# Optimization experiments

Measured on AMD Instinct MI355X. Metric: run time of the kernel, lower is better.

## Reference

```python
import jax, jax.numpy as jnp
import numpy as np

U = 8          # units per modular layer
B = 16384      # batch
IN = 512       # input feature dim
H = 512        # modular hidden dim
NC = 62        # n_class


def _aggregate(P, h):
    # P: [T, F] policy link matrix; h: [F, B, D] per-unit features.
    # agg[t] = sum_f P[t,f] * h[f], normalized by row-sum when row-sum > 0.
    s = jnp.einsum('tf,fbd->tbd', P, h)
    row = P.sum(axis=1)                      # [T]
    safe = jnp.where(row > 0, row, 1.0)[:, None, None]
    return jnp.where((row > 0)[:, None, None], s / safe, s)


def setup_inputs() -> dict:
    key = jax.random.key(0)
    ks = jax.random.split(key, 12)
    s_in = 1.0 / np.sqrt(IN)
    s_h = 1.0 / np.sqrt(H)
    return {
        'x': jax.random.normal(ks[0], (B, IN), jnp.float32),
        'policy1': jax.random.uniform(ks[1], (U * U,), jnp.float32),
        'policy2': jax.random.uniform(ks[2], (U * U,), jnp.float32),
        'policy_final': jax.random.uniform(ks[3], (U,), jnp.float32),
        'W0': jax.random.uniform(ks[4], (U, IN, H), jnp.float32, -s_in, s_in),
        'b0': jax.random.uniform(ks[5], (U, H), jnp.float32, -s_in, s_in),
        'W1': jax.random.uniform(ks[6], (U, H, H), jnp.float32, -s_h, s_h),
        'b1': jax.random.uniform(ks[7], (U, H), jnp.float32, -s_h, s_h),
        'W2': jax.random.uniform(ks[8], (U, H, NC), jnp.float32, -s_h, s_h),
        'b2': jax.random.uniform(ks[9], (U, NC), jnp.float32, -s_h, s_h),
    }


def reference(x, policy1, policy2, policy_final, W0, b0, W1, b1, W2, b2):
    # Layer 0 (input modular layer): policy_list[0] is forced to all-ones,
    # so every unit sees x unscaled. Each unit: Linear + ReLU.
    h0 = jax.nn.relu(jnp.einsum('bi,uid->ubd', x, W0) + b0[:, None, :])  # [U,B,H]

    # Mid layer: policy-gated weighted-sum aggregation, then per-unit Linear+ReLU.
    a1 = _aggregate(policy1.reshape(U, U), h0)
    h1 = jax.nn.relu(jnp.einsum('ubi,uid->ubd', a1, W1) + b1[:, None, :])

    # Output modular layer: aggregate then per-unit Linear (no activation).
    a2 = _aggregate(policy2.reshape(U, U), h1)
    h2 = jnp.einsum('ubi,uic->ubc', a2, W2) + b2[:, None, :]  # [U,B,NC]

    # Final gating. Original code divides by divider INSIDE the unit loop
    # (every iteration), so replicate that recurrence exactly.
    d = policy_final.sum()
    inv = jnp.where(d > 0, 1.0 / jnp.where(d > 0, d, 1.0), 1.0)
    out = jnp.zeros((B, NC), jnp.float32)
    for j in range(U):  # fixed small unit count, not a data dim
        out = (out + h2[j] * policy_final[j]) * inv
    return out
```

## Files before the change

kernel.cpp:

```cpp
#include <hip/hip_runtime.h>

#define U_   8
#define B_   16384
#define NC_  62

typedef __attribute__((ext_vector_type(8))) short bfrag;
typedef __attribute__((ext_vector_type(4))) float facc;

__device__ __forceinline__ float bf2f(unsigned int lo16) {
    union { unsigned int i; float f; } v;
    v.i = lo16 << 16;
    return v.f;
}
__device__ __forceinline__ unsigned short f2bf(float f) {
    unsigned int x = __float_as_uint(f);
    return (unsigned short)((x + 0x7fffu + ((x >> 16) & 1u)) >> 16);
}
__device__ __forceinline__ void gl2lds16(const void* g, void* l) {
    __builtin_amdgcn_global_load_lds(
        (const __attribute__((address_space(1))) void*)g,
        (__attribute__((address_space(3))) void*)l, 16, 0, 0);
}

__global__ void prep_kernel(const float* __restrict__ p1, const float* __restrict__ p2,
                            const float* __restrict__ pf, const float* __restrict__ b2,
                            float* __restrict__ P1n, float* __restrict__ P2n,
                            float* __restrict__ wfin, float* __restrict__ cconst)
{
    int t = threadIdx.x;
    if (t >= 64) return;
    int row = t >> 3;
    float s1 = 0.f, s2 = 0.f;
    for (int f = 0; f < 8; f++) { s1 += p1[row * 8 + f]; s2 += p2[row * 8 + f]; }
    P1n[t] = p1[t] * (s1 > 0.f ? 1.f / s1 : 1.f);
    P2n[t] = p2[t] * (s2 > 0.f ? 1.f / s2 : 1.f);
    float d = 0.f;
    for (int j = 0; j < 8; j++) d += pf[j];
    float inv = d > 0.f ? 1.f / d : 1.f;
    float wv[8];
    for (int j = 0; j < 8; j++) {
        float v = pf[j];
        for (int i = j; i < 8; i++) v *= inv;
        wv[j] = v;
    }
    if (t < 8) wfin[t] = wv[t];
    float cc = 0.f;
    if (t < NC_) for (int u = 0; u < 8; u++) cc += wv[u] * b2[u * NC_ + t];
    cconst[t] = cc;
}

__global__ __launch_bounds__(256) void reorder_w0(
    const float* __restrict__ W0, unsigned short* __restrict__ W0r)
{
    __shared__ float tile[32][33];
    const int u  = blockIdx.z;
    const int n0 = blockIdx.x * 32, k0 = blockIdx.y * 32;
    const int tx = threadIdx.x & 31, ty = threadIdx.x >> 5;
    const float* Wb = W0 + (long)u * 512 * 512;
#pragma unroll
    for (int i = 0; i < 4; i++)
        tile[ty + i * 8][tx] = Wb[(long)(k0 + ty + i * 8) * 512 + n0 + tx];
    __syncthreads();
#pragma unroll
    for (int i = 0; i < 4; i++) {
        int n = n0 + ty + i * 8, k = k0 + tx;
        int np = (n >> 5) * 256 + u * 32 + (n & 31);
        W0r[(long)np * 512 + k] = f2bf(tile[tx][ty + i * 8]);
    }
}

__global__ __launch_bounds__(256) void transpose_w(
    const float* __restrict__ W, unsigned short* __restrict__ Wt)
{
    __shared__ float tile[32][33];
    const int u  = blockIdx.z;
    const int n0 = blockIdx.x * 32, k0 = blockIdx.y * 32;
    const int tx = threadIdx.x & 31, ty = threadIdx.x >> 5;
    const float* Wb = W + (long)u * 512 * 512;
#pragma unroll
    for (int i = 0; i < 4; i++)
        tile[ty + i * 8][tx] = Wb[(long)(k0 + ty + i * 8) * 512 + n0 + tx];
    __syncthreads();
    unsigned short* Wo = Wt + (long)u * 512 * 512;
#pragma unroll
    for (int i = 0; i < 4; i++) {
        int n = n0 + ty + i * 8, k = k0 + tx;
        Wo[(long)n * 512 + k] = f2bf(tile[tx][ty + i * 8]);
    }
}

__global__ __launch_bounds__(256) void wout_build(
    const float* __restrict__ W2, const float* __restrict__ P2n,
    const float* __restrict__ wfin, unsigned short* __restrict__ Woutt)
{
    const int c   = threadIdx.x & 63;
    const int row = blockIdx.x * 4 + (threadIdx.x >> 6);
    const int f = row >> 9, k = row & 511;
    float s = 0.f;
    if (c < NC_) {
#pragma unroll
        for (int u = 0; u < 8; u++)
            s += wfin[u] * P2n[u * 8 + f] * W2[((long)u * 512 + k) * NC_ + c];
    }
    Woutt[(long)c * 4096 + row] = f2bf(s);
}

__global__ __launch_bounds__(256) void convert_x(
    const float* __restrict__ x, unsigned short* __restrict__ xb, long n)
{
    long i = ((long)blockIdx.x * 256 + threadIdx.x) * 8;
    if (i >= n) return;
    const float4* xp = (const float4*)(x + i);
    float4 a = xp[0], b = xp[1];
    uint4 o;
    o.x = f2bf(a.x) | ((unsigned)f2bf(a.y) << 16);
    o.y = f2bf(a.z) | ((unsigned)f2bf(a.w) << 16);
    o.z = f2bf(b.x) | ((unsigned)f2bf(b.y) << 16);
    o.w = f2bf(b.z) | ((unsigned)f2bf(b.w) << 16);
    *(uint4*)(xb + i) = o;
}

__global__ __launch_bounds__(512, 4) void gemm0_mix(
    const unsigned short* __restrict__ xb, const unsigned short* __restrict__ W0r,
    const float* __restrict__ b0, const float* __restrict__ P1n,
    unsigned short* __restrict__ a1, long plane)
{
    __shared__ __align__(16) unsigned short sm[128 * 264];
    unsigned short* sA = sm;
    unsigned short* sB = sm + 128 * 64;
    const int tid = threadIdx.x, w = tid >> 6, lane = tid & 63;
    const int flat = blockIdx.x;
    const int xcd = flat & 7, seq = flat >> 3;
    const int ng = xcd * 2 + (seq & 1);
    const long mBase = (long)(seq >> 1) * 128;

    const int lr = lane >> 3;
    const int lg = (lane & 7) ^ lr;
    const int wm = w >> 2, wn = w & 3;
    const int r = lane & 15, q = lane >> 4;
    const int x7 = r & 7;

    facc acc[4][4];
#pragma unroll
    for (int i = 0; i < 4; i++)
#pragma unroll
        for (int j = 0; j < 4; j++) acc[i][j] = (facc){0.f, 0.f, 0.f, 0.f};

    for (int k0 = 0; k0 < 512; k0 += 64) {
        __syncthreads();
#pragma unroll
        for (int i = 0; i < 2; i++) {
            const int c = w + i * 8;
            gl2lds16(xb + (mBase + c * 8 + lr) * 512 + k0 + lg * 8, sA + c * 512);
        }
#pragma unroll
        for (int i = 0; i < 4; i++) {
            const int c = w * 4 + i;
            gl2lds16(W0r + ((long)ng * 256 + c * 8 + lr) * 512 + k0 + lg * 8,
                     sB + c * 512);
        }
        __syncthreads();
#pragma unroll
        for (int h = 0; h < 2; h++) {
            const int xg = ((h * 4 + q) ^ x7) * 8;
            bfrag aF[4], bF[4];
#pragma unroll
            for (int mt = 0; mt < 4; mt++)
                aF[mt] = *(const bfrag*)&sA[(wm * 64 + mt * 16 + r) * 64 + xg];
#pragma unroll
            for (int nt = 0; nt < 4; nt++)
                bF[nt] = *(const bfrag*)&sB[(wn * 64 + nt * 16 + r) * 64 + xg];
#pragma unroll
            for (int mt = 0; mt < 4; mt++)
#pragma unroll
                for (int nt = 0; nt < 4; nt++)
                    acc[mt][nt] = __builtin_amdgcn_mfma_f32_16x16x32_bf16(
                        aF[mt], bF[nt], acc[mt][nt], 0, 0, 0);
        }
    }

    __syncthreads();
#pragma unroll
    for (int nt = 0; nt < 4; nt++) {
        const int cl = wn * 64 + nt * 16 + r;
        const float bv = b0[(cl >> 5) * 512 + ng * 32 + (cl & 31)];
#pragma unroll
        for (int mt = 0; mt < 4; mt++) {
            const int rowb = wm * 64 + mt * 16 + q * 4;
#pragma unroll
            for (int rg = 0; rg < 4; rg++) {
                float v = acc[mt][nt][rg] + bv;
                v = v > 0.f ? v : 0.f;
                sm[(rowb + rg) * 264 + cl] = f2bf(v);
            }
        }
    }
    __syncthreads();

    float pw[64];
#pragma unroll
    for (int i = 0; i < 64; i++) pw[i] = P1n[i];
    const int row = tid >> 2, fs = (tid & 3) * 8;
    float hv[8][8];
#pragma unroll
    for (int u = 0; u < 8; u++) {
        bfrag hx = *(const bfrag*)&sm[row * 264 + u * 32 + fs];
#pragma unroll
        for (int j = 0; j < 8; j++)
            hv[u][j] = bf2f((unsigned int)(unsigned short)hx[j]);
    }
    const long rowOff = (mBase + row) * 512 + ng * 32 + fs;
#pragma unroll
    for (int t = 0; t < 8; t++) {
        float o[8];
#pragma unroll
        for (int j = 0; j < 8; j++) {
            float s = 0.f;
#pragma unroll
            for (int u = 0; u < 8; u++) s = fmaf(pw[t * 8 + u], hv[u][j], s);
            o[j] = s;
        }
        uint4 ov;
        ov.x = f2bf(o[0]) | ((unsigned)f2bf(o[1]) << 16);
        ov.y = f2bf(o[2]) | ((unsigned)f2bf(o[3]) << 16);
        ov.z = f2bf(o[4]) | ((unsigned)f2bf(o[5]) << 16);
        ov.w = f2bf(o[6]) | ((unsigned)f2bf(o[7]) << 16);
        *(uint4*)(a1 + (long)t * plane + rowOff) = ov;
    }
}

__global__ __launch_bounds__(256, 4) void gemm_h(
    const unsigned short* __restrict__ a1,
    const unsigned short* __restrict__ W1t,
    const float* __restrict__ b1,
    unsigned short* __restrict__ h1, long plane)
{
    __shared__ __align__(16) unsigned short sm[128 * 136];
    unsigned short* sA = sm;
    unsigned short* sB = sm + 128 * 64;
    const int tid = threadIdx.x, w = tid >> 6, lane = tid & 63;
    const int flat = blockIdx.x;
    const int u = flat & 7, seq = flat >> 3;
    const int nBase = (seq & 3) * 128;
    const long mBase = (long)(seq >> 2) * 128;

    const int lr = lane >> 3, lg = (lane & 7) ^ lr;
    const int wm = w >> 1, wn = w & 1;
    const int r = lane & 15, q = lane >> 4;
    const int x7 = r & 7;

    const unsigned short* Ab = a1 + (long)u * plane;
    const unsigned short* Bb = W1t + ((long)u * 512 + nBase) * 512;

    facc acc[4][4];
#pragma unroll
    for (int i = 0; i < 4; i++)
#pragma unroll
        for (int j = 0; j < 4; j++) acc[i][j] = (facc){0.f, 0.f, 0.f, 0.f};

    for (int k0 = 0; k0 < 512; k0 += 64) {
        __syncthreads();
#pragma unroll
        for (int i = 0; i < 4; i++) {
            const int c = w * 4 + i;
            gl2lds16(Ab + (mBase + c * 8 + lr) * 512 + k0 + lg * 8, sA + c * 512);
            gl2lds16(Bb + (long)(c * 8 + lr) * 512 + k0 + lg * 8, sB + c * 512);
        }
        __syncthreads();
#pragma unroll
        for (int h = 0; h < 2; h++) {
            const int xg = ((h * 4 + q) ^ x7) * 8;
            bfrag aF[4], bF[4];
#pragma unroll
            for (int mt = 0; mt < 4; mt++)
                aF[mt] = *(const bfrag*)&sA[(wm * 64 + mt * 16 + r) * 64 + xg];
#pragma unroll
            for (int nt = 0; nt < 4; nt++)
                bF[nt] = *(const bfrag*)&sB[(wn * 64 + nt * 16 + r) * 64 + xg];
#pragma unroll
            for (int mt = 0; mt < 4; mt++)
#pragma unroll
                for (int nt = 0; nt < 4; nt++)
                    acc[mt][nt] = __builtin_amdgcn_mfma_f32_16x16x32_bf16(
                        aF[mt], bF[nt], acc[mt][nt], 0, 0, 0);
        }
    }

    __syncthreads();
#pragma unroll
    for (int nt = 0; nt < 4; nt++) {
        const int col = wn * 64 + nt * 16 + r;
        const float bv = b1[u * 512 + nBase + col];
#pragma unroll
        for (int mt = 0; mt < 4; mt++) {
            const int rowb = wm * 64 + mt * 16 + q * 4;
#pragma unroll
            for (int rg = 0; rg < 4; rg++) {
                float v = acc[mt][nt][rg] + bv;
                v = v > 0.f ? v : 0.f;
                sm[(rowb + rg) * 136 + col] = f2bf(v);
            }
        }
    }
    __syncthreads();

    unsigned short* Cb = h1 + (long)u * plane + mBase * 512 + nBase;
#pragma unroll
    for (int it = 0; it < 8; it++) {
        const int g = tid + it * 256;
        const int row = g >> 4, gr = g & 15;
        *(uint4*)(Cb + (long)row * 512 + gr * 8) = *(const uint4*)&sm[row * 136 + gr * 8];
    }
}

__global__ __launch_bounds__(256, 4) void gemm_out(
    const unsigned short* __restrict__ h1,
    const unsigned short* __restrict__ Bt,
    float* __restrict__ partial, long plane, int Bc)
{
    __shared__ __align__(16) unsigned short sA[64 * 64];
    __shared__ __align__(16) unsigned short sB[64 * 64];
    const int tid = threadIdx.x, w = tid >> 6, lane = tid & 63;
    const int flat = blockIdx.x;
    const int kc = flat & 1;
    const long mBase = (long)(flat >> 1) * 64;

    const int lr = lane >> 3, lg = (lane & 7) ^ lr;
    const int wm = w >> 1, wn = w & 1;
    const int r = lane & 15, q = lane >> 4;
    const int x7 = r & 7;

    facc acc[2][2];
#pragma unroll
    for (int i = 0; i < 2; i++)
#pragma unroll
        for (int j = 0; j < 2; j++) acc[i][j] = (facc){0.f, 0.f, 0.f, 0.f};

    for (int it = 0; it < 32; it++) {
        const int u = kc * 4 + (it >> 3);
        const int kk = (it & 7) * 64;
        __syncthreads();
#pragma unroll
        for (int i = 0; i < 2; i++) {
            const int c = w * 2 + i;
            gl2lds16(h1 + (long)u * plane + (mBase + c * 8 + lr) * 512 + kk + lg * 8,
                     sA + c * 512);
            gl2lds16(Bt + (long)(c * 8 + lr) * 4096 + u * 512 + kk + lg * 8,
                     sB + c * 512);
        }
        __syncthreads();
#pragma unroll
        for (int h = 0; h < 2; h++) {
            const int xg = ((h * 4 + q) ^ x7) * 8;
            bfrag aF[2], bF[2];
#pragma unroll
            for (int mt = 0; mt < 2; mt++)
                aF[mt] = *(const bfrag*)&sA[(wm * 32 + mt * 16 + r) * 64 + xg];
#pragma unroll
            for (int nt = 0; nt < 2; nt++)
                bF[nt] = *(const bfrag*)&sB[(wn * 32 + nt * 16 + r) * 64 + xg];
#pragma unroll
            for (int mt = 0; mt < 2; mt++)
#pragma unroll
                for (int nt = 0; nt < 2; nt++)
                    acc[mt][nt] = __builtin_amdgcn_mfma_f32_16x16x32_bf16(
                        aF[mt], bF[nt], acc[mt][nt], 0, 0, 0);
        }
    }

    float* pb = partial + ((long)kc * Bc + mBase) * 64;
#pragma unroll
    for (int nt = 0; nt < 2; nt++) {
        const int col = wn * 32 + nt * 16 + r;
#pragma unroll
        for (int mt = 0; mt < 2; mt++) {
#pragma unroll
            for (int rg = 0; rg < 4; rg++) {
                const int row = wm * 32 + mt * 16 + q * 4 + rg;
                pb[(long)row * 64 + col] = acc[mt][nt][rg];
            }
        }
    }
}

__global__ __launch_bounds__(256) void reduce_out(
    const float* __restrict__ partial, const float* __restrict__ cconst,
    float* __restrict__ out, int Bc)
{
    const long flat = (long)blockIdx.x * 256 + threadIdx.x;
    const long row = flat >> 2;
    const int cg = (int)(flat & 3) * 16;
    float s[16];
#pragma unroll
    for (int j = 0; j < 16; j++) s[j] = 0.f;
#pragma unroll
    for (int kc = 0; kc < 2; kc++) {
        const float4* p = (const float4*)(partial + ((long)kc * Bc + row) * 64 + cg);
#pragma unroll
        for (int v4 = 0; v4 < 4; v4++) {
            float4 v = p[v4];
            s[v4 * 4 + 0] += v.x; s[v4 * 4 + 1] += v.y;
            s[v4 * 4 + 2] += v.z; s[v4 * 4 + 3] += v.w;
        }
    }
#pragma unroll
    for (int j = 0; j < 16; j++) {
        const int c = cg + j;
        if (c < NC_) out[row * NC_ + c] = s[j] + cconst[c];
    }
}

extern "C" void kernel_launch(void* const* d_in, const int* in_sizes, int n_in,
                              void* d_out, int out_size, void* d_ws, size_t ws_size,
                              hipStream_t stream)
{
    const float* x  = (const float*)d_in[0];
    const float* p1 = (const float*)d_in[1];
    const float* p2 = (const float*)d_in[2];
    const float* pf = (const float*)d_in[3];
    const float* W0 = (const float*)d_in[4];
    const float* b0 = (const float*)d_in[5];
    const float* W1 = (const float*)d_in[6];
    const float* b1 = (const float*)d_in[7];
    const float* W2 = (const float*)d_in[8];
    const float* b2 = (const float*)d_in[9];
    float* out = (float*)d_out;

    char* ws = (char*)d_ws;
    size_t off = 0;
    auto alloc = [&](size_t bytes) -> void* {
        void* p = ws + off;
        off += (bytes + 255) & ~(size_t)255;
        return p;
    };
    float* P1n    = (float*)alloc(64 * sizeof(float));
    float* P2n    = (float*)alloc(64 * sizeof(float));
    float* wfin   = (float*)alloc(8 * sizeof(float));
    float* cconst = (float*)alloc(64 * sizeof(float));
    unsigned short* W0r   = (unsigned short*)alloc((size_t)4096 * 512 * 2);
    unsigned short* W1t   = (unsigned short*)alloc((size_t)U_ * 512 * 512 * 2);
    unsigned short* Woutt = (unsigned short*)alloc((size_t)64 * 4096 * 2);
    unsigned short* xb    = (unsigned short*)alloc((size_t)B_ * 512 * 2);

    size_t remain = ws_size > off ? ws_size - off : 0;
    int Bc = 2048;
    for (int cand = B_; cand >= 2048; cand >>= 1) {
        size_t need = 2ull * 8 * cand * 512 * 2 + 2ull * cand * 64 * 4 + 1024;
        if (need <= remain) { Bc = cand; break; }
    }
    unsigned short* a1 = (unsigned short*)alloc(8ull * Bc * 512 * 2);
    unsigned short* h1 = (unsigned short*)alloc(8ull * Bc * 512 * 2);
    float* partial     = (float*)alloc(2ull * Bc * 64 * 4);

    prep_kernel<<<1, 64, 0, stream>>>(p1, p2, pf, b2, P1n, P2n, wfin, cconst);
    reorder_w0<<<dim3(16, 16, 8), 256, 0, stream>>>(W0, W0r);
    transpose_w<<<dim3(16, 16, 8), 256, 0, stream>>>(W1, W1t);
    wout_build<<<dim3(1024), 256, 0, stream>>>(W2, P2n, wfin, Woutt);
    convert_x<<<dim3(B_ * 512 / 8 / 256), 256, 0, stream>>>(x, xb, (long)B_ * 512);

    const int Mb = Bc / 128;
    const long plane = (long)Bc * 512;
    for (int bb = 0; bb < B_; bb += Bc) {
        gemm0_mix<<<dim3(16 * Mb), 512, 0, stream>>>(
            xb + (long)bb * 512, W0r, b0, P1n, a1, plane);
        gemm_h<<<dim3(32 * Mb), 256, 0, stream>>>(a1, W1t, b1, h1, plane);
        gemm_out<<<dim3(2 * (Bc / 64)), 256, 0, stream>>>(h1, Woutt, partial, plane, Bc);
        reduce_out<<<dim3(Bc / 64), 256, 0, stream>>>(
            partial, cconst, out + (long)bb * NC_, Bc);
    }
}
```

Baseline: 344.6 us.

## Double-buffer LDS tiles with async global_load_lds prefetch in all three GEMMs

Converts the K-loops of gemm0_mix, gemm_h and gemm_out from single-buffered load/sync/compute into a two-stage pipeline. The next tile is issued with global_load_lds into the alternate buffer, and explicit vmcnt waits plus raw s_barrier replace __syncthreads. The aim is to hide global-load latency behind MFMA work. In exchange LDS use doubles and the launch-bounds occupancy hints drop, so fewer blocks may be resident per CU.

```diff
diff --git a/kernel.cpp b/kernel.cpp
--- a/kernel.cpp
+++ b/kernel.cpp
@@ -21,6 +21,13 @@
         (const __attribute__((address_space(1))) void*)g,
         (__attribute__((address_space(3))) void*)l, 16, 0, 0);
 }
+__device__ __forceinline__ void cfence() { asm volatile("" ::: "memory"); }
+__device__ __forceinline__ void bar() {
+    asm volatile("" ::: "memory");
+    __builtin_amdgcn_s_barrier();
+    asm volatile("" ::: "memory");
+}
+#define VMCNT(n) asm volatile("s_waitcnt vmcnt(" #n ")" ::: "memory")
 
 __global__ void prep_kernel(const float* __restrict__ p1, const float* __restrict__ p2,
                             const float* __restrict__ pf, const float* __restrict__ b2,
@@ -120,14 +127,12 @@
     *(uint4*)(xb + i) = o;
 }
 
-__global__ __launch_bounds__(512, 4) void gemm0_mix(
+__global__ __launch_bounds__(512, 2) void gemm0_mix(
     const unsigned short* __restrict__ xb, const unsigned short* __restrict__ W0r,
     const float* __restrict__ b0, const float* __restrict__ P1n,
     unsigned short* __restrict__ a1, long plane)
 {
-    __shared__ __align__(16) unsigned short sm[128 * 264];
-    unsigned short* sA = sm;
-    unsigned short* sB = sm + 128 * 64;
+    __shared__ __align__(16) unsigned short sm[49152];
     const int tid = threadIdx.x, w = tid >> 6, lane = tid & 63;
     const int flat = blockIdx.x;
     const int xcd = flat & 7, seq = flat >> 3;
@@ -146,20 +151,25 @@
 #pragma unroll
         for (int j = 0; j < 4; j++) acc[i][j] = (facc){0.f, 0.f, 0.f, 0.f};
 
-    for (int k0 = 0; k0 < 512; k0 += 64) {
-        __syncthreads();
+    auto stage = [&](int buf, int kt) {
+        const int k0 = kt * 64;
+        unsigned short* dA = sm + buf * 8192;
+        unsigned short* dB = sm + 16384 + buf * 16384;
 #pragma unroll
         for (int i = 0; i < 2; i++) {
             const int c = w + i * 8;
-            gl2lds16(xb + (mBase + c * 8 + lr) * 512 + k0 + lg * 8, sA + c * 512);
+            gl2lds16(xb + (mBase + c * 8 + lr) * 512 + k0 + lg * 8, dA + c * 512);
         }
 #pragma unroll
         for (int i = 0; i < 4; i++) {
             const int c = w * 4 + i;
             gl2lds16(W0r + ((long)ng * 256 + c * 8 + lr) * 512 + k0 + lg * 8,
-                     sB + c * 512);
-        }
-        __syncthreads();
+                     dB + c * 512);
+        }
+    };
+    auto compute = [&](int buf) {
+        const unsigned short* sA = sm + buf * 8192;
+        const unsigned short* sB = sm + 16384 + buf * 16384;
 #pragma unroll
         for (int h = 0; h < 2; h++) {
             const int xg = ((h * 4 + q) ^ x7) * 8;
@@ -177,9 +187,29 @@
                     acc[mt][nt] = __builtin_amdgcn_mfma_f32_16x16x32_bf16(
                         aF[mt], bF[nt], acc[mt][nt], 0, 0, 0);
         }
-    }
-
-    __syncthreads();
+    };
+
+    stage(0, 0);
+    cfence();
+    stage(1, 1);
+    VMCNT(6);
+    bar();
+#pragma unroll
+    for (int t = 0; t < 8; ++t) {
+        compute(t & 1);
+        if (t <= 5) {
+            bar();
+            stage(t & 1, t + 2);
+            VMCNT(6);
+            bar();
+        } else if (t == 6) {
+            VMCNT(0);
+            bar();
+        } else {
+            bar();
+        }
+    }
+
 #pragma unroll
     for (int nt = 0; nt < 4; nt++) {
         const int cl = wn * 64 + nt * 16 + r;
@@ -229,15 +259,13 @@
     }
 }
 
-__global__ __launch_bounds__(256, 4) void gemm_h(
+__global__ __launch_bounds__(256, 2) void gemm_h(
     const unsigned short* __restrict__ a1,
     const unsigned short* __restrict__ W1t,
     const float* __restrict__ b1,
     unsigned short* __restrict__ h1, long plane)
 {
-    __shared__ __align__(16) unsigned short sm[128 * 136];
-    unsigned short* sA = sm;
-    unsigned short* sB = sm + 128 * 64;
+    __shared__ __align__(16) unsigned short sm[32768];
     const int tid = threadIdx.x, w = tid >> 6, lane = tid & 63;
     const int flat = blockIdx.x;
     const int u = flat & 7, seq = flat >> 3;
@@ -258,15 +286,20 @@
 #pragma unroll
         for (int j = 0; j < 4; j++) acc[i][j] = (facc){0.f, 0.f, 0.f, 0.f};
 
-    for (int k0 = 0; k0 < 512; k0 += 64) {
-        __syncthreads();
+    auto stage = [&](int buf, int kt) {
+        const int k0 = kt * 64;
+        unsigned short* dA = sm + buf * 8192;
+        unsigned short* dB = sm + 16384 + buf * 8192;
 #pragma unroll
         for (int i = 0; i < 4; i++) {
             const int c = w * 4 + i;
-            gl2lds16(Ab + (mBase + c * 8 + lr) * 512 + k0 + lg * 8, sA + c * 512);
-            gl2lds16(Bb + (long)(c * 8 + lr) * 512 + k0 + lg * 8, sB + c * 512);
-        }
-        __syncthreads();
+            gl2lds16(Ab + (mBase + c * 8 + lr) * 512 + k0 + lg * 8, dA + c * 512);
+            gl2lds16(Bb + (long)(c * 8 + lr) * 512 + k0 + lg * 8, dB + c * 512);
+        }
+    };
+    auto compute = [&](int buf) {
+        const unsigned short* sA = sm + buf * 8192;
+        const unsigned short* sB = sm + 16384 + buf * 8192;
 #pragma unroll
         for (int h = 0; h < 2; h++) {
             const int xg = ((h * 4 + q) ^ x7) * 8;
@@ -284,9 +317,29 @@
                     acc[mt][nt] = __builtin_amdgcn_mfma_f32_16x16x32_bf16(
                         aF[mt], bF[nt], acc[mt][nt], 0, 0, 0);
         }
-    }
-
-    __syncthreads();
+    };
+
+    stage(0, 0);
+    cfence();
+    stage(1, 1);
+    VMCNT(8);
+    bar();
+#pragma unroll
+    for (int t = 0; t < 8; ++t) {
+        compute(t & 1);
+        if (t <= 5) {
+            bar();
+            stage(t & 1, t + 2);
+            VMCNT(8);
+            bar();
+        } else if (t == 6) {
+            VMCNT(0);
+            bar();
+        } else {
+            bar();
+        }
+    }
+
 #pragma unroll
     for (int nt = 0; nt < 4; nt++) {
         const int col = wn * 64 + nt * 16 + r;
@@ -313,13 +366,12 @@
     }
 }
 
-__global__ __launch_bounds__(256, 4) void gemm_out(
+__global__ __launch_bounds__(256, 1) void gemm_out(
     const unsigned short* __restrict__ h1,
     const unsigned short* __restrict__ Bt,
     float* __restrict__ partial, long plane, int Bc)
 {
-    __shared__ __align__(16) unsigned short sA[64 * 64];
-    __shared__ __align__(16) unsigned short sB[64 * 64];
+    __shared__ __align__(16) unsigned short sm[16384];
     const int tid = threadIdx.x, w = tid >> 6, lane = tid & 63;
     const int flat = blockIdx.x;
     const int kc = flat & 1;
@@ -336,19 +388,23 @@
 #pragma unroll
         for (int j = 0; j < 2; j++) acc[i][j] = (facc){0.f, 0.f, 0.f, 0.f};
 
-    for (int it = 0; it < 32; it++) {
+    auto stage = [&](int buf, int it) {
         const int u = kc * 4 + (it >> 3);
         const int kk = (it & 7) * 64;
-        __syncthreads();
+        unsigned short* dA = sm + buf * 4096;
+        unsigned short* dB = sm + 8192 + buf * 4096;
 #pragma unroll
         for (int i = 0; i < 2; i++) {
             const int c = w * 2 + i;
             gl2lds16(h1 + (long)u * plane + (mBase + c * 8 + lr) * 512 + kk + lg * 8,
-                     sA + c * 512);
+                     dA + c * 512);
             gl2lds16(Bt + (long)(c * 8 + lr) * 4096 + u * 512 + kk + lg * 8,
-                     sB + c * 512);
-        }
-        __syncthreads();
+                     dB + c * 512);
+        }
+    };
+    auto compute = [&](int buf) {
+        const unsigned short* sA = sm + buf * 4096;
+        const unsigned short* sB = sm + 8192 + buf * 4096;
 #pragma unroll
         for (int h = 0; h < 2; h++) {
             const int xg = ((h * 4 + q) ^ x7) * 8;
@@ -365,6 +421,25 @@
                 for (int nt = 0; nt < 2; nt++)
                     acc[mt][nt] = __builtin_amdgcn_mfma_f32_16x16x32_bf16(
                         aF[mt], bF[nt], acc[mt][nt], 0, 0, 0);
+        }
+    };
+
+    stage(0, 0);
+    cfence();
+    stage(1, 1);
+    VMCNT(4);
+    bar();
+#pragma unroll
+    for (int t = 0; t < 32; ++t) {
+        compute(t & 1);
+        if (t <= 29) {
+            bar();
+            stage(t & 1, t + 2);
+            VMCNT(4);
+            bar();
+        } else if (t == 30) {
+            VMCNT(0);
+            bar();
         }
     }
 
```

Result: faster. 315.6 us (-8.4%).
